# Kernel optimization log

Measured on AMD Instinct MI355X. Metric: run time of the kernel, lower is better.

The kernel has to match this reference:

```python
import jax, jax.numpy as jnp
import numpy as np

N_NODES = 50000
N_EDGES = 800000
IN_CH, HID_CH, OUT_CH = 128, 256, 128


def setup_inputs() -> dict:
    key = jax.random.key(0)
    ks = jax.random.split(key, 9)
    x = jax.random.normal(ks[0], (N_NODES, IN_CH), dtype=jnp.float32)
    edge_index = jax.random.randint(ks[1], (2, N_EDGES), 0, N_NODES, dtype=jnp.int64)
    # SAGEConv params: lin_l (aggregated neighbors, with bias), lin_r (root, no bias)
    s1 = 1.0 / np.sqrt(IN_CH)
    s2 = 1.0 / np.sqrt(HID_CH)
    W1_l = jax.random.uniform(ks[2], (IN_CH, HID_CH), jnp.float32, -s1, s1)
    W1_r = jax.random.uniform(ks[3], (IN_CH, HID_CH), jnp.float32, -s1, s1)
    b1 = jax.random.uniform(ks[4], (HID_CH,), jnp.float32, -s1, s1)
    W2_l = jax.random.uniform(ks[5], (HID_CH, OUT_CH), jnp.float32, -s2, s2)
    W2_r = jax.random.uniform(ks[6], (HID_CH, OUT_CH), jnp.float32, -s2, s2)
    b2 = jax.random.uniform(ks[7], (OUT_CH,), jnp.float32, -s2, s2)
    return {"x": x, "edge_index": edge_index, "W1_l": W1_l, "W1_r": W1_r,
            "b1": b1, "W2_l": W2_l, "W2_r": W2_r, "b2": b2}


def _sage_conv(x, edge_index, Wl, Wr, b):
    # PyG SAGEConv: out = lin_l(mean_{j in N(i)} x_j) + lin_r(x_i)
    src, dst = edge_index[0], edge_index[1]
    msg = x[src]                                                    # [E, C] gather
    agg = jax.ops.segment_sum(msg, dst, num_segments=x.shape[0])    # [N, C] scatter-add
    cnt = jax.ops.segment_sum(jnp.ones((src.shape[0],), x.dtype), dst,
                              num_segments=x.shape[0])              # [N]
    agg = agg / jnp.maximum(cnt, 1.0)[:, None]                      # mean; deg-0 -> 0
    return agg @ Wl + x @ Wr + b


def reference(x, edge_index, W1_l, W1_r, b1, W2_l, W2_r, b2):
    h = jax.nn.relu(_sage_conv(x, edge_index, W1_l, W1_r, b1))
    # dropout(p=0.5) is stochastic; use eval-mode identity for a deterministic baseline
    out = _sage_conv(h, edge_index, W2_l, W2_r, b2)
    return jax.nn.log_softmax(out, axis=1)
```

## Files before the change

### kernel.cpp

```cpp
#include <hip/hip_runtime.h>
#include <math.h>

#define NN 50000
#define NE 800000
#define BINW 256
#define NB ((NN + BINW - 1) / BINW)
#define CAP 4864
#define CHUNK 4096
#define NBIN ((NE + CHUNK - 1) / CHUNK)
#define NXB 6250
#define NWB 256
#define EPT 16

typedef __attribute__((ext_vector_type(8))) _Float16 f16x8;
typedef __attribute__((ext_vector_type(2))) _Float16 h2;
typedef __attribute__((ext_vector_type(4))) float f32x4;
typedef unsigned int uint32;
typedef __attribute__((address_space(3))) unsigned int lds_uint;
typedef const __attribute__((address_space(1))) unsigned int glb_uint;

__device__ inline unsigned short f2h(float f) {
    _Float16 h = (_Float16)f;
    return __builtin_bit_cast(unsigned short, h);
}
__device__ inline uint32 pack2h(float a, float b) {
    return (uint32)f2h(a) | ((uint32)f2h(b) << 16);
}
__device__ inline h2 as_h2(uint32 u) { return __builtin_bit_cast(h2, u); }

__device__ inline int edge_at(const void* edges, int is64, int i) {
    return is64 ? (int)((const long long*)edges)[i] : ((const int*)edges)[i];
}

__global__ __launch_bounds__(256)
void k_front(const void* __restrict__ edges, uint32* __restrict__ gbuf,
             int* __restrict__ bcnt,
             const float* __restrict__ x, unsigned short* __restrict__ A1,
             const float* __restrict__ W1l, const float* __restrict__ W1r,
             const float* __restrict__ W2l, const float* __restrict__ W2r,
             unsigned short* __restrict__ B1t, unsigned short* __restrict__ B2t) {
    int b = blockIdx.x;
    if (b >= NBIN) {
        if (b < NBIN + NXB) {
            int t = (b - NBIN) * 256 + threadIdx.x;
            if (t >= NN * 32) return;
            int node = t >> 5, q = t & 31;
            float4 v = *(const float4*)(x + (size_t)node * 128 + q * 4);
            *(uint2*)(A1 + (size_t)node * 256 + 128 + q * 4) =
                make_uint2(pack2h(v.x, v.y), pack2h(v.z, v.w));
        } else {
            int t = (b - NBIN - NXB) * 256 + threadIdx.x;
            int n = t >> 8, k = t & 255;
            float v1 = (k < 128) ? W1l[k * 256 + n] : W1r[(k - 128) * 256 + n];
            B1t[n * 256 + k] = f2h(v1);
            float v2 = (n < 128) ? W2l[k * 128 + n] : W2r[k * 128 + (n - 128)];
            B2t[n * 256 + k] = f2h(v2);
        }
        return;
    }
    __shared__ int hist[NB], excl[NB], cur[NB], gpos[NB];
    __shared__ int is64s;
    __shared__ uint32 sorted[CHUNK];
    int t = threadIdx.x;
    int base = b * CHUNK;
    int n = NE - base; if (n > CHUNK) n = CHUNK;
    if (t < 64) {
        const long long* q = (const long long*)edges;
        long long v = q[t];
        unsigned long long m = __ballot(v >= 0 && v < NN);
        if (t == 0) is64s = (m == ~0ull) ? 1 : 0;
    }
    for (int i = t; i < NB; i += 256) hist[i] = 0;
    __syncthreads();
    int is64 = is64s;
    int sA[EPT], dA[EPT];
    #pragma unroll
    for (int q = 0; q < EPT; ++q) {
        int i = t + q * 256;
        if (i < n) {
            sA[q] = edge_at(edges, is64, base + i);
            dA[q] = edge_at(edges, is64, NE + base + i);
        } else dA[q] = -1;
    }
    #pragma unroll
    for (int q = 0; q < EPT; ++q)
        if (dA[q] >= 0) atomicAdd(&hist[dA[q] >> 8], 1);
    __syncthreads();
    if (t == 0) {
        int s = 0;
        for (int k = 0; k < NB; ++k) { excl[k] = s; s += hist[k]; }
    }
    __syncthreads();
    for (int i = t; i < NB; i += 256) {
        gpos[i] = atomicAdd(&bcnt[i], hist[i]);
        cur[i] = excl[i];
    }
    __syncthreads();
    #pragma unroll
    for (int q = 0; q < EPT; ++q) {
        if (dA[q] >= 0) {
            int bk = dA[q] >> 8;
            int lp = atomicAdd(&cur[bk], 1);
            sorted[lp] = ((uint32)bk << 24) | ((uint32)(dA[q] & (BINW - 1)) << 16) | (uint32)sA[q];
        }
    }
    __syncthreads();
    for (int i = t; i < n; i += 256) {
        uint32 v = sorted[i];
        int bk = v >> 24;
        int gp = gpos[bk] + (i - excl[bk]);
        if (gp < CAP) gbuf[(size_t)bk * CAP + gp] = v & 0xFFFFFFu;
    }
}

__global__ __launch_bounds__(256) void k_sort(const uint32* __restrict__ gbuf,
                                              const int* __restrict__ bcnt,
                                              int* __restrict__ offs,
                                              unsigned short* __restrict__ ssrc) {
    __shared__ int hist[BINW], cur[BINW], wsum[4];
    __shared__ int sorted[CAP];
    __shared__ int bb_s;
    int b = blockIdx.x, t = threadIdx.x;
    int lane = t & 63, w = t >> 6;
    int c = (t < NB) ? bcnt[t] : 0;
    int pre = (t < b) ? c : 0;
    #pragma unroll
    for (int s = 1; s < 64; s <<= 1) pre += __shfl_xor(pre, s);
    if (lane == 0) wsum[w] = pre;
    hist[t] = 0;
    __syncthreads();
    if (t == 0) bb_s = wsum[0] + wsum[1] + wsum[2] + wsum[3];
    __syncthreads();
    int bb = bb_s;
    int cnt = bcnt[b]; if (cnt > CAP) cnt = CAP;
    int nbase = b * BINW;
    int ncnt = NN - nbase; if (ncnt > BINW) ncnt = BINW;
    for (int i = t; i < cnt; i += 256)
        atomicAdd(&hist[gbuf[(size_t)b * CAP + i] >> 16], 1);
    __syncthreads();
    int d = hist[t];
    int v = d;
    #pragma unroll
    for (int s = 1; s < 64; s <<= 1) { int x = __shfl_up(v, s); if (lane >= s) v += x; }
    if (lane == 63) wsum[w] = v;
    __syncthreads();
    if (t == 0) { int s = 0; for (int i = 0; i < 4; ++i) { int x = wsum[i]; wsum[i] = s; s += x; } }
    __syncthreads();
    int excl = wsum[w] + (v - d);
    if (t < ncnt) offs[nbase + t] = bb + excl;
    if (b == NB - 1 && t == 0) offs[NN] = NE;
    cur[t] = excl;
    __syncthreads();
    for (int i = t; i < cnt; i += 256) {
        uint32 p = gbuf[(size_t)b * CAP + i];
        int lp = atomicAdd(&cur[p >> 16], 1);
        sorted[lp] = (int)(p & 0xFFFFu);
    }
    __syncthreads();
    for (int i = t; i < cnt; i += 256)
        ssrc[bb + i] = (unsigned short)sorted[i];
}

#define ACCH1(vv) { a[0] += as_h2((vv).x); a[1] += as_h2((vv).y); \
                    a[2] += as_h2((vv).z); a[3] += as_h2((vv).w); }

__device__ inline void group_gather(const unsigned short* __restrict__ tab, int coff,
                                    const unsigned short* __restrict__ ssrc,
                                    int s0, int deg, int md, int grp, int lig, h2* a) {
    const unsigned short* bp = tab + coff + lig * 8;
    int idxA = (lig < deg)      ? (int)ssrc[s0 + lig]      : 0;
    int idxB = (16 + lig < deg) ? (int)ssrc[s0 + 16 + lig] : 0;
    int cap = md < 32 ? md : 32;
    for (int i0 = 0; i0 < cap; i0 += 8) {
        uint4 v[8];
        #pragma unroll
        for (int u = 0; u < 8; ++u) {
            int i = i0 + u;
            int word = (i & 16) ? idxB : idxA;
            int s = __shfl(word, grp * 16 + (i & 15));
            v[u] = *(const uint4*)(bp + (size_t)s * 256);
        }
        #pragma unroll
        for (int u = 0; u < 8; ++u) if (i0 + u < deg) ACCH1(v[u]);
    }
    for (int i0 = 32; i0 < md; i0 += 4) {
        uint4 v[4];
        #pragma unroll
        for (int u = 0; u < 4; ++u) {
            int i = i0 + u;
            int s = (i < deg) ? (int)ssrc[s0 + i] : 0;
            v[u] = *(const uint4*)(bp + (size_t)s * 256);
        }
        #pragma unroll
        for (int u = 0; u < 4; ++u) if (i0 + u < deg) ACCH1(v[u]);
    }
}

__global__ void k_agg(unsigned short* __restrict__ A1, const int* __restrict__ offs,
                      const unsigned short* __restrict__ ssrc) {
    int lane = threadIdx.x & 63;
    int grp = lane >> 4, lig = lane & 15;
    int wid = (blockIdx.x * 256 + threadIdx.x) >> 6;
    int node = wid * 4 + grp;
    int s0 = offs[node], deg = offs[node + 1] - s0;
    int md = deg;
    md = max(md, __shfl_xor(md, 16));
    md = max(md, __shfl_xor(md, 32));
    h2 a[4] = {};
    group_gather(A1, 128, ssrc, s0, deg, md, grp, lig, a);
    float inv = 1.0f / fmaxf((float)deg, 1.0f);
    uint4 p;
    p.x = pack2h((float)a[0][0] * inv, (float)a[0][1] * inv);
    p.y = pack2h((float)a[1][0] * inv, (float)a[1][1] * inv);
    p.z = pack2h((float)a[2][0] * inv, (float)a[2][1] * inv);
    p.w = pack2h((float)a[3][0] * inv, (float)a[3][1] * inv);
    *(uint4*)(A1 + (size_t)node * 256 + lig * 8) = p;
}

template <bool RELU>
__global__ __launch_bounds__(256)
void k_gemm_bf(const unsigned short* __restrict__ A, const unsigned short* __restrict__ Bt,
               const float* __restrict__ bias, unsigned short* __restrict__ C) {
    __shared__ unsigned short AsmL[3][128 * 32];
    __shared__ unsigned short BsmL[3][128 * 32];
    int t = threadIdx.x;
    int lane = t & 63, w = t >> 6;
    int m0 = blockIdx.x * 128, n0 = blockIdx.y * 128;
    int wr = (w >> 1) * 64, wc = (w & 1) * 64;
    int fr = lane & 15, fk = (lane >> 4) * 8;

    f32x4 acc[4][4] = {};
    int srow = lane >> 2;
    int scol = (lane & 3) * 8;
    auto STAGE = [&](int bufi, int ks) {
        #pragma unroll
        for (int q = 0; q < 2; ++q) {
            int widx = w * 2 + q;
            int row = widx * 16 + srow;
            const unsigned short* ga = A + (size_t)(m0 + row) * 256 + ks * 32 + scol;
            __builtin_amdgcn_global_load_lds((glb_uint*)ga, (lds_uint*)&AsmL[bufi][widx * 512], 16, 0, 0);
            const unsigned short* gb = Bt + (size_t)(n0 + row) * 256 + ks * 32 + scol;
            __builtin_amdgcn_global_load_lds((glb_uint*)gb, (lds_uint*)&BsmL[bufi][widx * 512], 16, 0, 0);
        }
    };

    STAGE(0, 0);
    STAGE(1, 1);
    #pragma unroll
    for (int ks = 0; ks < 8; ++ks) {
        if (ks < 7) asm volatile("s_waitcnt vmcnt(4)" ::: "memory");
        else        asm volatile("s_waitcnt vmcnt(0)" ::: "memory");
        __builtin_amdgcn_s_barrier();
        __builtin_amdgcn_sched_barrier(0);
        if (ks < 6) STAGE((ks + 2) % 3, ks + 2);
        int cb = ks % 3;
        f16x8 af[4], bfr[4];
        #pragma unroll
        for (int i = 0; i < 4; ++i) af[i] = *(const f16x8*)&AsmL[cb][(wr + i * 16 + fr) * 32 + fk];
        #pragma unroll
        for (int j = 0; j < 4; ++j) bfr[j] = *(const f16x8*)&BsmL[cb][(wc + j * 16 + fr) * 32 + fk];
        #pragma unroll
        for (int i = 0; i < 4; ++i)
            #pragma unroll
            for (int j = 0; j < 4; ++j)
                acc[i][j] = __builtin_amdgcn_mfma_f32_16x16x32_f16(af[i], bfr[j], acc[i][j], 0, 0, 0);
    }

    int r0 = (lane >> 4) * 4;
    #pragma unroll
    for (int i = 0; i < 4; ++i) {
        #pragma unroll
        for (int j = 0; j < 4; ++j) {
            int gn = n0 + wc + j * 16 + fr;
            float bb = RELU ? bias[gn] : 0.f;
            #pragma unroll
            for (int rr = 0; rr < 4; ++rr) {
                int gm = m0 + wr + i * 16 + r0 + rr;
                if (gm >= NN) continue;
                float v = acc[i][j][rr];
                if (RELU) v = fmaxf(v + bb, 0.f);
                C[(size_t)gm * 256 + gn] = f2h(v);
            }
        }
    }
}

__global__ void k_final(const unsigned short* __restrict__ P, const int* __restrict__ offs,
                        const unsigned short* __restrict__ ssrc, const float* __restrict__ b2,
                        float* __restrict__ out) {
    int lane = threadIdx.x & 63;
    int grp = lane >> 4, lig = lane & 15;
    int wid = (blockIdx.x * 256 + threadIdx.x) >> 6;
    int node = wid * 4 + grp;
    int s0 = offs[node], deg = offs[node + 1] - s0;
    int md = deg;
    md = max(md, __shfl_xor(md, 16));
    md = max(md, __shfl_xor(md, 32));
    h2 a[4] = {};
    group_gather(P, 0, ssrc, s0, deg, md, grp, lig, a);
    float inv = 1.0f / fmaxf((float)deg, 1.0f);
    uint4 rv = *(const uint4*)(P + (size_t)node * 256 + 128 + lig * 8);
    float4 ba = *(const float4*)(b2 + lig * 8);
    float4 bb = *(const float4*)(b2 + lig * 8 + 4);
    h2 r0 = as_h2(rv.x), r1 = as_h2(rv.y), r2 = as_h2(rv.z), r3 = as_h2(rv.w);
    float vv[8];
    vv[0] = (float)a[0][0] * inv + (float)r0[0] + ba.x;
    vv[1] = (float)a[0][1] * inv + (float)r0[1] + ba.y;
    vv[2] = (float)a[1][0] * inv + (float)r1[0] + ba.z;
    vv[3] = (float)a[1][1] * inv + (float)r1[1] + ba.w;
    vv[4] = (float)a[2][0] * inv + (float)r2[0] + bb.x;
    vv[5] = (float)a[2][1] * inv + (float)r2[1] + bb.y;
    vv[6] = (float)a[3][0] * inv + (float)r3[0] + bb.z;
    vv[7] = (float)a[3][1] * inv + (float)r3[1] + bb.w;

    float mx = vv[0];
    #pragma unroll
    for (int k = 1; k < 8; ++k) mx = fmaxf(mx, vv[k]);
    #pragma unroll
    for (int d = 1; d < 16; d <<= 1) mx = fmaxf(mx, __shfl_xor(mx, d));
    float s = 0.f;
    #pragma unroll
    for (int k = 0; k < 8; ++k) s += __expf(vv[k] - mx);
    #pragma unroll
    for (int d = 1; d < 16; d <<= 1) s += __shfl_xor(s, d);
    float ls = logf(s);
    float4 o0 = make_float4(vv[0] - mx - ls, vv[1] - mx - ls, vv[2] - mx - ls, vv[3] - mx - ls);
    float4 o1 = make_float4(vv[4] - mx - ls, vv[5] - mx - ls, vv[6] - mx - ls, vv[7] - mx - ls);
    *(float4*)(out + (size_t)node * 128 + lig * 8) = o0;
    *(float4*)(out + (size_t)node * 128 + lig * 8 + 4) = o1;
}

extern "C" void kernel_launch(void* const* d_in, const int* in_sizes, int n_in,
                              void* d_out, int out_size, void* d_ws, size_t ws_size,
                              hipStream_t stream) {
    const float* x   = (const float*)d_in[0];
    const void*  edg = d_in[1];
    const float* W1l = (const float*)d_in[2];
    const float* W1r = (const float*)d_in[3];
    const float* b1  = (const float*)d_in[4];
    const float* W2l = (const float*)d_in[5];
    const float* W2r = (const float*)d_in[6];
    const float* b2  = (const float*)d_in[7];
    float* out = (float*)d_out;

    char* ws = (char*)d_ws;
    size_t off = 0;
    auto alloc = [&](size_t bytes) {
        size_t cur = off;
        off = (off + bytes + 255) & ~(size_t)255;
        return cur;
    };
    int* bcnt  = (int*)(ws + alloc((size_t)NB * 4));
    int* offs  = (int*)(ws + alloc((size_t)(NN + 1) * 4));
    unsigned short* ssrc = (unsigned short*)(ws + alloc((size_t)NE * 2));
    uint32* gbuf = (uint32*)(ws + alloc((size_t)NB * CAP * 4));
    unsigned short* A1  = (unsigned short*)(ws + alloc((size_t)NN * 256 * 2));
    unsigned short* Hb  = (unsigned short*)(ws + alloc((size_t)NN * 256 * 2));
    unsigned short* Pb  = (unsigned short*)(ws + alloc((size_t)NN * 256 * 2));
    unsigned short* B1t = (unsigned short*)(ws + alloc((size_t)65536 * 2));
    unsigned short* B2t = (unsigned short*)(ws + alloc((size_t)65536 * 2));
    (void)alloc(65536);

    int nb_g = NN / 16;
    int mblocks = (NN + 127) / 128;

    hipMemsetAsync(bcnt, 0, (size_t)NB * 4, stream);
    k_front<<<NBIN + NXB + NWB, 256, 0, stream>>>(edg, gbuf, bcnt, x, A1,
                                                  W1l, W1r, W2l, W2r, B1t, B2t);
    k_sort<<<NB, 256, 0, stream>>>(gbuf, bcnt, offs, ssrc);
    k_agg<<<nb_g, 256, 0, stream>>>(A1, offs, ssrc);
    k_gemm_bf<true><<<dim3(mblocks, 2), 256, 0, stream>>>(A1, B1t, b1, Hb);
    k_gemm_bf<false><<<dim3(mblocks, 2), 256, 0, stream>>>(Hb, B2t, nullptr, Pb);
    k_final<<<nb_g, 256, 0, stream>>>(Pb, offs, ssrc, b2, out);
}
```

Baseline: 137.0 us.

## Gather neighbor features as FP8 e4m3 to halve gather bandwidth

Adds an FP8 (e4m3) copy of the input features and of the layer-2 neighbor projection, written in the front kernel and the second GEMM epilogue. Both neighbor-gather kernels now read 8 bytes per lane instead of 16 and decode to fp16 with bit tricks before accumulating. The goal is to cut the random-gather memory traffic that dominates aggregation. In exchange it adds software encode cost and a large precision loss (3-bit mantissa), which risks failing accuracy tolerance.

Result: slower. 155.2 us (+13.3%).

```diff
diff --git a/kernel.cpp b/kernel.cpp
--- a/kernel.cpp
+++ b/kernel.cpp
@@ -28,6 +28,38 @@
 }
 __device__ inline h2 as_h2(uint32 u) { return __builtin_bit_cast(h2, u); }
 
+__device__ inline uint32 f2e4m3(float f) {
+    unsigned short h = f2h(f);
+    uint32 s = (h >> 8) & 0x80u;
+    int E = (h >> 10) & 0x1F;
+    int M = h & 0x3FF;
+    if (E >= 24) return s | 0x7Eu;
+    if (E > 8) {
+        int m = M >> 7, r = M & 0x7F;
+        if (r > 0x40 || (r == 0x40 && (m & 1))) { m++; if (m == 8) { m = 0; E++; if (E >= 24) return s | 0x7Eu; } }
+        return s | (uint32)((E - 8) << 3) | (uint32)m;
+    }
+    if (E < 5) return s;
+    int sh = 16 - E;
+    int t = 1024 + M;
+    int m = t >> sh;
+    int rem = t & ((1 << sh) - 1);
+    int half = 1 << (sh - 1);
+    if (rem > half || (rem == half && (m & 1))) m++;
+    if (m >= 8) return s | 0x08u;
+    return s | (uint32)m;
+}
+
+__device__ inline void dec_acc(uint32 w, h2* a) {
+    uint32 u01 = (w & 0x7Fu) | ((w & 0x7F00u) << 8);
+    uint32 u23 = ((w >> 16) & 0x7Fu) | ((w >> 8) & 0x7F0000u);
+    uint32 h01 = ((u01 << 7) + 0x20002000u) | ((w & 0x80u) << 8) | ((w & 0x8000u) << 16);
+    uint32 h23 = ((u23 << 7) + 0x20002000u) | ((w >> 8) & 0x8000u) | (w & 0x80000000u);
+    a[0] += as_h2(h01);
+    a[1] += as_h2(h23);
+}
+#define ACC8Q(vv) { dec_acc((vv).x, a); dec_acc((vv).y, a + 2); }
+
 __device__ inline int edge_at(const void* edges, int is64, int i) {
     return is64 ? (int)((const long long*)edges)[i] : ((const int*)edges)[i];
 }
@@ -36,6 +68,7 @@
 void k_front(const void* __restrict__ edges, uint32* __restrict__ gbuf,
              int* __restrict__ bcnt,
              const float* __restrict__ x, unsigned short* __restrict__ A1,
+             uint32* __restrict__ x8w,
              const float* __restrict__ W1l, const float* __restrict__ W1r,
              const float* __restrict__ W2l, const float* __restrict__ W2r,
              unsigned short* __restrict__ B1t, unsigned short* __restrict__ B2t) {
@@ -48,6 +81,8 @@
             float4 v = *(const float4*)(x + (size_t)node * 128 + q * 4);
             *(uint2*)(A1 + (size_t)node * 256 + 128 + q * 4) =
                 make_uint2(pack2h(v.x, v.y), pack2h(v.z, v.w));
+            x8w[(size_t)node * 32 + q] = f2e4m3(v.x) | (f2e4m3(v.y) << 8) |
+                                         (f2e4m3(v.z) << 16) | (f2e4m3(v.w) << 24);
         } else {
             int t = (b - NBIN - NXB) * 256 + threadIdx.x;
             int n = t >> 8, k = t & 255;
@@ -161,43 +196,40 @@
         ssrc[bb + i] = (unsigned short)sorted[i];
 }
 
-#define ACCH1(vv) { a[0] += as_h2((vv).x); a[1] += as_h2((vv).y); \
-                    a[2] += as_h2((vv).z); a[3] += as_h2((vv).w); }
-
-__device__ inline void group_gather(const unsigned short* __restrict__ tab, int coff,
-                                    const unsigned short* __restrict__ ssrc,
-                                    int s0, int deg, int md, int grp, int lig, h2* a) {
-    const unsigned short* bp = tab + coff + lig * 8;
+__device__ inline void group_gather8(const unsigned char* __restrict__ tab,
+                                     const unsigned short* __restrict__ ssrc,
+                                     int s0, int deg, int md, int grp, int lig, h2* a) {
+    const unsigned char* bp = tab + lig * 8;
     int idxA = (lig < deg)      ? (int)ssrc[s0 + lig]      : 0;
     int idxB = (16 + lig < deg) ? (int)ssrc[s0 + 16 + lig] : 0;
     int cap = md < 32 ? md : 32;
     for (int i0 = 0; i0 < cap; i0 += 8) {
-        uint4 v[8];
+        uint2 v[8];
         #pragma unroll
         for (int u = 0; u < 8; ++u) {
             int i = i0 + u;
             int word = (i & 16) ? idxB : idxA;
             int s = __shfl(word, grp * 16 + (i & 15));
-            v[u] = *(const uint4*)(bp + (size_t)s * 256);
-        }
-        #pragma unroll
-        for (int u = 0; u < 8; ++u) if (i0 + u < deg) ACCH1(v[u]);
+            v[u] = *(const uint2*)(bp + (size_t)s * 128);
+        }
+        #pragma unroll
+        for (int u = 0; u < 8; ++u) if (i0 + u < deg) ACC8Q(v[u]);
     }
     for (int i0 = 32; i0 < md; i0 += 4) {
-        uint4 v[4];
+        uint2 v[4];
         #pragma unroll
         for (int u = 0; u < 4; ++u) {
             int i = i0 + u;
             int s = (i < deg) ? (int)ssrc[s0 + i] : 0;
-            v[u] = *(const uint4*)(bp + (size_t)s * 256);
-        }
-        #pragma unroll
-        for (int u = 0; u < 4; ++u) if (i0 + u < deg) ACCH1(v[u]);
-    }
-}
-
-__global__ void k_agg(unsigned short* __restrict__ A1, const int* __restrict__ offs,
-                      const unsigned short* __restrict__ ssrc) {
+            v[u] = *(const uint2*)(bp + (size_t)s * 128);
+        }
+        #pragma unroll
+        for (int u = 0; u < 4; ++u) if (i0 + u < deg) ACC8Q(v[u]);
+    }
+}
+
+__global__ void k_agg(unsigned short* __restrict__ A1, const unsigned char* __restrict__ x8,
+                      const int* __restrict__ offs, const unsigned short* __restrict__ ssrc) {
     int lane = threadIdx.x & 63;
     int grp = lane >> 4, lig = lane & 15;
     int wid = (blockIdx.x * 256 + threadIdx.x) >> 6;
@@ -207,7 +239,7 @@
     md = max(md, __shfl_xor(md, 16));
     md = max(md, __shfl_xor(md, 32));
     h2 a[4] = {};
-    group_gather(A1, 128, ssrc, s0, deg, md, grp, lig, a);
+    group_gather8(x8, ssrc, s0, deg, md, grp, lig, a);
     float inv = 1.0f / fmaxf((float)deg, 1.0f);
     uint4 p;
     p.x = pack2h((float)a[0][0] * inv, (float)a[0][1] * inv);
@@ -217,10 +249,11 @@
     *(uint4*)(A1 + (size_t)node * 256 + lig * 8) = p;
 }
 
-template <bool RELU>
+template <bool RELU, bool SPLIT>
 __global__ __launch_bounds__(256)
 void k_gemm_bf(const unsigned short* __restrict__ A, const unsigned short* __restrict__ Bt,
-               const float* __restrict__ bias, unsigned short* __restrict__ C) {
+               const float* __restrict__ bias, unsigned short* __restrict__ C,
+               unsigned char* __restrict__ p8, unsigned short* __restrict__ r16) {
     __shared__ unsigned short AsmL[3][128 * 32];
     __shared__ unsigned short BsmL[3][128 * 32];
     int t = threadIdx.x;
@@ -279,15 +312,22 @@
                 if (gm >= NN) continue;
                 float v = acc[i][j][rr];
                 if (RELU) v = fmaxf(v + bb, 0.f);
-                C[(size_t)gm * 256 + gn] = f2h(v);
+                if (!SPLIT) {
+                    C[(size_t)gm * 256 + gn] = f2h(v);
+                } else {
+                    if (gn < 128) p8[(size_t)gm * 128 + gn] = (unsigned char)f2e4m3(v);
+                    else          r16[(size_t)gm * 128 + gn - 128] = f2h(v);
+                }
             }
         }
     }
 }
 
-__global__ void k_final(const unsigned short* __restrict__ P, const int* __restrict__ offs,
-                        const unsigned short* __restrict__ ssrc, const float* __restrict__ b2,
-                        float* __restrict__ out) {
+__global__ void k_final(const unsigned char* __restrict__ p8,
+                        const unsigned short* __restrict__ r16,
+                        const int* __restrict__ offs,
+                        const unsigned short* __restrict__ ssrc,
+                        const float* __restrict__ b2, float* __restrict__ out) {
     int lane = threadIdx.x & 63;
     int grp = lane >> 4, lig = lane & 15;
     int wid = (blockIdx.x * 256 + threadIdx.x) >> 6;
@@ -297,9 +337,9 @@
     md = max(md, __shfl_xor(md, 16));
     md = max(md, __shfl_xor(md, 32));
     h2 a[4] = {};
-    group_gather(P, 0, ssrc, s0, deg, md, grp, lig, a);
+    group_gather8(p8, ssrc, s0, deg, md, grp, lig, a);
     float inv = 1.0f / fmaxf((float)deg, 1.0f);
-    uint4 rv = *(const uint4*)(P + (size_t)node * 256 + 128 + lig * 8);
+    uint4 rv = *(const uint4*)(r16 + (size_t)node * 128 + lig * 8);
     float4 ba = *(const float4*)(b2 + lig * 8);
     float4 bb = *(const float4*)(b2 + lig * 8 + 4);
     h2 r0 = as_h2(rv.x), r1 = as_h2(rv.y), r2 = as_h2(rv.z), r3 = as_h2(rv.w);
@@ -356,7 +396,9 @@
     uint32* gbuf = (uint32*)(ws + alloc((size_t)NB * CAP * 4));
     unsigned short* A1  = (unsigned short*)(ws + alloc((size_t)NN * 256 * 2));
     unsigned short* Hb  = (unsigned short*)(ws + alloc((size_t)NN * 256 * 2));
-    unsigned short* Pb  = (unsigned short*)(ws + alloc((size_t)NN * 256 * 2));
+    unsigned char*  x8  = (unsigned char*)(ws + alloc((size_t)NN * 128));
+    unsigned char*  p8  = (unsigned char*)(ws + alloc((size_t)NN * 128));
+    unsigned short* r16 = (unsigned short*)(ws + alloc((size_t)NN * 128 * 2));
     unsigned short* B1t = (unsigned short*)(ws + alloc((size_t)65536 * 2));
     unsigned short* B2t = (unsigned short*)(ws + alloc((size_t)65536 * 2));
     (void)alloc(65536);
@@ -365,11 +407,11 @@
     int mblocks = (NN + 127) / 128;
 
     hipMemsetAsync(bcnt, 0, (size_t)NB * 4, stream);
-    k_front<<<NBIN + NXB + NWB, 256, 0, stream>>>(edg, gbuf, bcnt, x, A1,
+    k_front<<<NBIN + NXB + NWB, 256, 0, stream>>>(edg, gbuf, bcnt, x, A1, (uint32*)x8,
                                                   W1l, W1r, W2l, W2r, B1t, B2t);
     k_sort<<<NB, 256, 0, stream>>>(gbuf, bcnt, offs, ssrc);
-    k_agg<<<nb_g, 256, 0, stream>>>(A1, offs, ssrc);
-    k_gemm_bf<true><<<dim3(mblocks, 2), 256, 0, stream>>>(A1, B1t, b1, Hb);
-    k_gemm_bf<false><<<dim3(mblocks, 2), 256, 0, stream>>>(Hb, B2t, nullptr, Pb);
-    k_final<<<nb_g, 256, 0, stream>>>(Pb, offs, ssrc, b2, out);
-}
+    k_agg<<<nb_g, 256, 0, stream>>>(A1, x8, offs, ssrc);
+    k_gemm_bf<true, false><<<dim3(mblocks, 2), 256, 0, stream>>>(A1, B1t, b1, Hb, nullptr, nullptr);
+    k_gemm_bf<false, true><<<dim3(mblocks, 2), 256, 0, stream>>>(Hb, B2t, nullptr, nullptr, p8, r16);
+    k_final<<<nb_g, 256, 0, stream>>>(p8, r16, offs, ssrc, b2, out);
+}
```
